# Performance work log

Measured on AMD Instinct MI355X. Metric: run time of the kernel, lower is better.

Reference implementation:

```python
import jax, jax.numpy as jnp
import numpy as np

B, S, DIM = 2, 2048, 1024
HID = 2048          # multiple_of-rounded hidden dim
E, NSH, TOPK = 8, 2, 2


def _ffn(x, w1, w2, w3):
    return (jax.nn.silu(x @ w1.T) * (x @ w3.T)) @ w2.T


def setup_inputs() -> dict:
    key = jax.random.key(0)
    ks = jax.random.split(key, 8)
    sc = 0.02  # init scale for stability
    return {
        "x": jax.random.normal(ks[0], (B, S, DIM), jnp.float32),
        "router_w": jax.random.normal(ks[1], (E, DIM), jnp.float32) * sc,
        "expert_bias": jnp.zeros((E,), jnp.float32),
        "w1": jax.random.normal(ks[2], (E, HID, DIM), jnp.float32) * sc,
        "w3": jax.random.normal(ks[3], (E, HID, DIM), jnp.float32) * sc,
        "w2": jax.random.normal(ks[4], (E, DIM, HID), jnp.float32) * sc,
        "sw1": jax.random.normal(ks[5], (NSH, HID, DIM), jnp.float32) * sc,
        "sw3": jax.random.normal(ks[6], (NSH, HID, DIM), jnp.float32) * sc,
        "sw2": jax.random.normal(ks[7], (NSH, DIM, HID), jnp.float32) * sc,
    }


def reference(x, router_w, expert_bias, w1, w3, w2, sw1, sw3, sw2):
    bs, sl, d = x.shape
    xf = x.reshape(-1, d)  # [T, d]

    # shared experts (always-on)
    shared = jnp.zeros_like(xf)
    for i in range(sw1.shape[0]):
        shared = shared + _ffn(xf, sw1[i], sw2[i], sw3[i])

    # router with aux-free load-balance bias
    logits = xf @ router_w.T + expert_bias  # [T, E]
    rw, sel = jax.lax.top_k(logits, TOPK)   # [T, K]
    rw = jax.nn.softmax(rw.astype(jnp.float32), axis=-1).astype(x.dtype)

    # combine weights per (token, expert): sum of routing weights over topk slots
    onehot = jax.nn.one_hot(sel, E, dtype=x.dtype)        # [T, K, E]
    combine = jnp.einsum('tk,tke->te', rw, onehot)        # [T, E]

    # per-expert FFN accumulated via scan (equivalent to gather-FFN-scatter)
    def body(acc, ew):
        e1, e3, e2, cw = ew  # cw: [T]
        acc = acc + cw[:, None] * _ffn(xf, e1, e2, e3)
        return acc, None

    out, _ = jax.lax.scan(body, jnp.zeros_like(xf), (w1, w3, w2, combine.T))
    out = out + shared
    return out.reshape(bs, sl, -1)
```

## Files before the change

### kernel.cpp

```cpp
#include <hip/hip_runtime.h>
#include <stdint.h>

#define T_TOK 4096
#define DIMD  1024
#define HIDN  2048
#define NEXP  8
#define RMAX  10240
#define RROWS (RMAX + 2 * T_TOK)

typedef float f32x4 __attribute__((ext_vector_type(4)));
typedef short s16x8 __attribute__((ext_vector_type(8)));

__device__ __forceinline__ uint16_t f2bf(float f) {
    uint32_t u = __builtin_bit_cast(uint32_t, f);
    u += 0x7fffu + ((u >> 16) & 1u);
    return (uint16_t)(u >> 16);
}
__device__ __forceinline__ float bf2f(uint32_t h) {
    return __builtin_bit_cast(float, h << 16);
}
__device__ __forceinline__ uint32_t pk2(float a, float b) {
    return (uint32_t)f2bf(a) | ((uint32_t)f2bf(b) << 16);
}
__device__ __forceinline__ void gload16(const void* g, void* l) {
    __builtin_amdgcn_global_load_lds(
        (const __attribute__((address_space(1))) void*)g,
        (__attribute__((address_space(3))) void*)l, 16, 0, 0);
}
#define BAR()        asm volatile("s_barrier" ::: "memory")
#define WAIT_VM4()   asm volatile("s_waitcnt vmcnt(4)" ::: "memory")
#define WAIT_VM0()   asm volatile("s_waitcnt vmcnt(0)" ::: "memory")
#define WAIT_LGKM0() asm volatile("s_waitcnt lgkmcnt(0)" ::: "memory")


struct CvtArgs {
    const float* s[7];
    uint16_t*    d[7];
    int          nq[7];
    int          mode[7];
};

__global__ void cvt_all_kernel(CvtArgs a) {
    int base = blockIdx.x * blockDim.x + threadIdx.x;
    int stride = gridDim.x * blockDim.x;
    #pragma unroll
    for (int seg = 0; seg < 7; ++seg) {
        const float4* sp = (const float4*)a.s[seg];
        uint2* dp = (uint2*)a.d[seg];
        int n = a.nq[seg];
        int mode = a.mode[seg];
        for (int i = base; i < n; i += stride) {
            float4 v = sp[i];
            uint2 o; o.x = pk2(v.x, v.y); o.y = pk2(v.z, v.w);
            int di = i;
            if (mode) {
                int e = i >> 19;
                int rem = i & 524287;
                int nr = rem >> 8;
                int kq = rem & 255;
                int np = ((nr >> 4) << 5) + ((mode == 2) ? 16 : 0) + (nr & 15);
                di = (e << 20) + (np << 8) + kq;
            }
            dp[di] = o;
        }
    }
}

__global__ __launch_bounds__(256)
void router_kernel(const float* __restrict__ x, const float* __restrict__ rw,
                   const float* __restrict__ bias,
                   int* __restrict__ sel, float* __restrict__ wgt,
                   int* __restrict__ cnt) {
    __shared__ float rws[NEXP * DIMD];
    int tid = threadIdx.x;
    for (int i = tid; i < NEXP * DIMD / 4; i += 256)
        ((float4*)rws)[i] = ((const float4*)rw)[i];
    __syncthreads();

    int wid = tid >> 6, lane = tid & 63;
    float b[NEXP];
    #pragma unroll
    for (int e = 0; e < NEXP; ++e) b[e] = bias[e];

    int t0 = (blockIdx.x * 4 + wid) * 8;
    for (int j = 0; j < 8; ++j) {
        int t = t0 + j;
        const float4* xr = (const float4*)(x + (size_t)t * DIMD);
        float p[NEXP] = {};
        #pragma unroll
        for (int c = 0; c < 4; ++c) {
            float4 xv = xr[c * 64 + lane];
            #pragma unroll
            for (int e = 0; e < NEXP; ++e) {
                float4 wv = *(const float4*)(rws + e * DIMD + c * 256 + lane * 4);
                p[e] += xv.x * wv.x + xv.y * wv.y + xv.z * wv.z + xv.w * wv.w;
            }
        }
        #pragma unroll
        for (int off = 32; off >= 1; off >>= 1) {
            #pragma unroll
            for (int e = 0; e < NEXP; ++e) p[e] += __shfl_xor(p[e], off, 64);
        }
        if (lane == 0) {
            #pragma unroll
            for (int e = 0; e < NEXP; ++e) p[e] += b[e];
            float l0 = -1e30f; int i0 = 0;
            #pragma unroll
            for (int e = 0; e < NEXP; ++e) { if (p[e] > l0) { l0 = p[e]; i0 = e; } }
            float l1 = -1e30f; int i1 = 0;
            #pragma unroll
            for (int e = 0; e < NEXP; ++e) { if (e == i0) continue; if (p[e] > l1) { l1 = p[e]; i1 = e; } }
            float e1 = expf(l1 - l0);
            float d = 1.f + e1;
            sel[t * 2] = i0; sel[t * 2 + 1] = i1;
            wgt[t * 2] = 1.f / d; wgt[t * 2 + 1] = e1 / d;
            atomicAdd(&cnt[i0], 1);
            atomicAdd(&cnt[i1], 1);
        }
    }
}

__global__ void offs_kernel(const int* __restrict__ cnt, int* __restrict__ offs) {
    if (threadIdx.x == 0 && blockIdx.x == 0) {
        int o = 0;
        for (int e = 0; e < NEXP; ++e) { offs[e] = o; o += (cnt[e] + 255) & ~255; }
        offs[NEXP] = o;
    }
}

__global__ void assign_kernel(const int* __restrict__ sel, const int* __restrict__ offs,
                              int* __restrict__ fill, int* __restrict__ row_of,
                              int* __restrict__ tok) {
    int i = blockIdx.x * blockDim.x + threadIdx.x;
    if (i < 2 * T_TOK) {
        int e = sel[i];
        int r = offs[e] + atomicAdd(&fill[e], 1);
        row_of[i] = r;
        tok[r] = i >> 1;
    } else if (i < 4 * T_TOK) {
        int j = i - 2 * T_TOK;
        tok[offs[NEXP] + j] = j & (T_TOK - 1);
    }
}

__global__ void combine_kernel(const uint16_t* __restrict__ H2, const int* __restrict__ row_of,
                               const float* __restrict__ wgt, const int* __restrict__ offs,
                               float* __restrict__ out) {
    int t = blockIdx.x;
    int c = threadIdx.x * 8;
    int r0 = row_of[t * 2], r1 = row_of[t * 2 + 1];
    int s0 = offs[NEXP] + t, s1 = s0 + T_TOK;
    float w0 = wgt[t * 2], w1 = wgt[t * 2 + 1];
    uint4 a = *(const uint4*)(H2 + (size_t)r0 * DIMD + c);
    uint4 b = *(const uint4*)(H2 + (size_t)r1 * DIMD + c);
    uint4 u = *(const uint4*)(H2 + (size_t)s0 * DIMD + c);
    uint4 v = *(const uint4*)(H2 + (size_t)s1 * DIMD + c);
    float4 o0, o1;
    o0.x = w0 * bf2f(a.x & 0xffffu) + w1 * bf2f(b.x & 0xffffu) + bf2f(u.x & 0xffffu) + bf2f(v.x & 0xffffu);
    o0.y = w0 * bf2f(a.x >> 16)     + w1 * bf2f(b.x >> 16)     + bf2f(u.x >> 16)     + bf2f(v.x >> 16);
    o0.z = w0 * bf2f(a.y & 0xffffu) + w1 * bf2f(b.y & 0xffffu) + bf2f(u.y & 0xffffu) + bf2f(v.y & 0xffffu);
    o0.w = w0 * bf2f(a.y >> 16)     + w1 * bf2f(b.y >> 16)     + bf2f(u.y >> 16)     + bf2f(v.y >> 16);
    o1.x = w0 * bf2f(a.z & 0xffffu) + w1 * bf2f(b.z & 0xffffu) + bf2f(u.z & 0xffffu) + bf2f(v.z & 0xffffu);
    o1.y = w0 * bf2f(a.z >> 16)     + w1 * bf2f(b.z >> 16)     + bf2f(u.z >> 16)     + bf2f(v.z >> 16);
    o1.z = w0 * bf2f(a.w & 0xffffu) + w1 * bf2f(b.w & 0xffffu) + bf2f(u.w & 0xffffu) + bf2f(v.w & 0xffffu);
    o1.w = w0 * bf2f(a.w >> 16)     + w1 * bf2f(b.w >> 16)     + bf2f(u.w >> 16)     + bf2f(v.w >> 16);
    float* o = out + (size_t)t * DIMD + c;
    *(float4*)o = o0;
    *(float4*)(o + 4) = o1;
}

__global__ __launch_bounds__(512, 2)
void gemm13_8p(const uint16_t* __restrict__ A, const int* __restrict__ tok,
               const uint16_t* __restrict__ W, uint16_t* __restrict__ H,
               const int* __restrict__ offs) {
    constexpr int K = DIMD;
    constexpr int NT = K / 64;
    __shared__ __align__(16) char lds[131072];

    int row0 = blockIdx.y * 256;
    int rsh = row0 - offs[NEXP];
    int e;
    if (rsh >= 0) {
        if (rsh >= 2 * T_TOK) return;
        e = NEXP + (rsh >> 12);
    } else {
        e = 0;
        while (row0 >= offs[e + 1]) ++e;
    }
    const uint16_t* wp = W + (size_t)e * (4096ull * 1024ull);
    int col0 = blockIdx.x * 256;

    int tid = threadIdx.x, lane = tid & 63, wid = tid >> 6;
    int wm = wid >> 2, wn = wid & 3;

    int sslot = (lane & 3) ^ ((tid >> 3) & 3);
    uint32_t aoff[2], boff[2];
    #pragma unroll
    for (int i = 0; i < 2; ++i) {
        int r = i * 128 + (tid >> 2);
        int garow = tok[row0 + r];
        aoff[i] = (uint32_t)garow * K + sslot * 8;
        boff[i] = (uint32_t)(col0 + r) * K + sslot * 8;
    }
    int ldsw = wid * 1024;

    int rslot = (((lane >> 4) ^ ((lane >> 1) & 3)) << 4);
    int aro = (wm * 128 + (lane & 15)) * 64 + rslot;
    int bro = (wn * 64 + (lane & 15)) * 64 + rslot;

    #define STAGE_A(buf, kt, ks) { \
        gload16(A + aoff[0] + (kt) + (ks) * 32, (buf) + (ks) * 16384 + ldsw); \
        gload16(A + aoff[1] + (kt) + (ks) * 32, (buf) + (ks) * 16384 + 8192 + ldsw); }
    #define STAGE_B(buf, kt, ks) { \
        gload16(wp + boff[0] + (kt) + (ks) * 32, (buf) + 32768 + (ks) * 16384 + ldsw); \
        gload16(wp + boff[1] + (kt) + (ks) * 32, (buf) + 32768 + (ks) * 16384 + 8192 + ldsw); }

    STAGE_A(lds, 0, 0); STAGE_B(lds, 0, 0);
    STAGE_A(lds, 0, 1); STAGE_B(lds, 0, 1);
    WAIT_VM4();
    BAR();

    f32x4 acc[8][4] = {};

    for (int t = 0; t < NT; ++t) {
        char* cur = lds + (t & 1) * 65536;
        char* nxt = lds + ((t + 1) & 1) * 65536;
        int kt1 = (t + 1) * 64;
        bool pre = (t + 1 < NT);
        s16x8 av[4], bv[4], av2[4];

        #pragma unroll
        for (int f = 0; f < 4; ++f) av[f] = *(const s16x8*)(cur + aro + f * 1024);
        #pragma unroll
        for (int f = 0; f < 4; ++f) bv[f] = *(const s16x8*)(cur + 32768 + bro + f * 1024);
        if (pre) STAGE_A(nxt, kt1, 0);
        BAR(); WAIT_LGKM0();
        __builtin_amdgcn_s_setprio(1);
        #pragma unroll
        for (int j = 0; j < 4; ++j)
            #pragma unroll
            for (int i = 0; i < 4; ++i)
                acc[i][j] = __builtin_amdgcn_mfma_f32_16x16x32_bf16(av[i], bv[j], acc[i][j], 0, 0, 0);
        __builtin_amdgcn_s_setprio(0);
        BAR();

        #pragma unroll
        for (int f = 0; f < 4; ++f) av2[f] = *(const s16x8*)(cur + aro + (f + 4) * 1024);
        if (pre) STAGE_B(nxt, kt1, 0);
        BAR(); WAIT_LGKM0();
        __builtin_amdgcn_s_setprio(1);
        #pragma unroll
        for (int j = 0; j < 4; ++j)
            #pragma unroll
            for (int i = 0; i < 4; ++i)
                acc[i + 4][j] = __builtin_amdgcn_mfma_f32_16x16x32_bf16(av2[i], bv[j], acc[i + 4][j], 0, 0, 0);
        __builtin_amdgcn_s_setprio(0);
        if (pre) { WAIT_VM4(); } else { WAIT_VM0(); }
        BAR();

        #pragma unroll
        for (int f = 0; f < 4; ++f) av[f] = *(const s16x8*)(cur + 16384 + aro + f * 1024);
        #pragma unroll
        for (int f = 0; f < 4; ++f) bv[f] = *(const s16x8*)(cur + 32768 + 16384 + bro + f * 1024);
        if (pre) STAGE_A(nxt, kt1, 1);
        BAR(); WAIT_LGKM0();
        __builtin_amdgcn_s_setprio(1);
        #pragma unroll
        for (int j = 0; j < 4; ++j)
            #pragma unroll
            for (int i = 0; i < 4; ++i)
                acc[i][j] = __builtin_amdgcn_mfma_f32_16x16x32_bf16(av[i], bv[j], acc[i][j], 0, 0, 0);
        __builtin_amdgcn_s_setprio(0);
        BAR();

        #pragma unroll
        for (int f = 0; f < 4; ++f) av2[f] = *(const s16x8*)(cur + 16384 + aro + (f + 4) * 1024);
        if (pre) STAGE_B(nxt, kt1, 1);
        BAR(); WAIT_LGKM0();
        __builtin_amdgcn_s_setprio(1);
        #pragma unroll
        for (int j = 0; j < 4; ++j)
            #pragma unroll
            for (int i = 0; i < 4; ++i)
                acc[i + 4][j] = __builtin_amdgcn_mfma_f32_16x16x32_bf16(av2[i], bv[j], acc[i + 4][j], 0, 0, 0);
        __builtin_amdgcn_s_setprio(0);
        if (pre) WAIT_VM4();
        BAR();
    }
    #undef STAGE_A
    #undef STAGE_B

    #pragma unroll
    for (int i = 0; i < 8; ++i) {
        int row = row0 + wm * 128 + i * 16 + ((lane >> 4) << 2);
        #pragma unroll
        for (int m = 0; m < 2; ++m) {
            int hc = ((col0 + wn * 64) >> 1) + m * 16 + (lane & 15);
            #pragma unroll
            for (int rg = 0; rg < 4; ++rg) {
                float a1 = acc[i][2 * m][rg];
                float a3 = acc[i][2 * m + 1][rg];
                float hv = (a1 / (1.f + __expf(-a1))) * a3;
                H[(size_t)(row + rg) * HIDN + hc] = f2bf(hv);
            }
        }
    }
}

__global__ __launch_bounds__(256, 2)
void gemm2_2p(const uint16_t* __restrict__ Hg,
              const uint16_t* __restrict__ W2, uint16_t* __restrict__ H2,
              const int* __restrict__ offs) {
    constexpr int K = HIDN;
    constexpr int NT = K / 64;
    __shared__ __align__(16) char lds[65536];

    int row0 = blockIdx.y * 128;
    int rsh = row0 - offs[NEXP];
    int e;
    if (rsh >= 0) {
        if (rsh >= 2 * T_TOK) return;
        e = NEXP + (rsh >> 12);
    } else {
        e = 0;
        while (row0 >= offs[e + 1]) ++e;
    }
    const uint16_t* wp = W2 + (size_t)e * DIMD * HIDN;
    int col0 = blockIdx.x * 128;

    int tid = threadIdx.x, lane = tid & 63, wid = tid >> 6;
    int wm = wid >> 1, wn = wid & 1;

    int chunk = (tid & 3) ^ ((tid >> 3) & 3);
    uint32_t aoff[2], boff[2];
    #pragma unroll
    for (int p = 0; p < 2; ++p) {
        int r = p * 64 + (tid >> 2);
        aoff[p] = (uint32_t)(row0 + r) * K + chunk * 8;
        boff[p] = (uint32_t)(col0 + r) * K + chunk * 8;
    }
    int ldsw = wid * 1024;

    int rslot = (((lane >> 4) ^ ((lane >> 1) & 3)) << 4);
    int aro = (wm * 64 + (lane & 15)) * 64 + rslot;
    int bro = (wn * 64 + (lane & 15)) * 64 + rslot + 16384;

    #define STG_A2(buf, kt, ks) { \
        gload16(Hg + aoff[0] + (kt) + (ks) * 32, (buf) + (ks) * 8192 + ldsw); \
        gload16(Hg + aoff[1] + (kt) + (ks) * 32, (buf) + (ks) * 8192 + 4096 + ldsw); }
    #define STG_B2(buf, kt, ks) { \
        gload16(wp + boff[0] + (kt) + (ks) * 32, (buf) + 16384 + (ks) * 8192 + ldsw); \
        gload16(wp + boff[1] + (kt) + (ks) * 32, (buf) + 16384 + (ks) * 8192 + 4096 + ldsw); }

    STG_A2(lds, 0, 0); STG_B2(lds, 0, 0);
    STG_A2(lds, 0, 1); STG_B2(lds, 0, 1);
    WAIT_VM4();
    BAR();

    f32x4 acc[4][4] = {};

    for (int t = 0; t < NT; ++t) {
        char* cur = lds + (t & 1) * 32768;
        char* nxt = lds + ((t + 1) & 1) * 32768;
        int kt1 = (t + 1) * 64;
        bool pre = (t + 1 < NT);
        s16x8 av[4], bv[4];

        #pragma unroll
        for (int f = 0; f < 4; ++f) av[f] = *(const s16x8*)(cur + aro + f * 1024);
        #pragma unroll
        for (int f = 0; f < 4; ++f) bv[f] = *(const s16x8*)(cur + bro + f * 1024);
        if (pre) { STG_A2(nxt, kt1, 0); STG_B2(nxt, kt1, 0); }
        BAR(); WAIT_LGKM0();
        __builtin_amdgcn_s_setprio(1);
        #pragma unroll
        for (int j = 0; j < 4; ++j)
            #pragma unroll
            for (int i = 0; i < 4; ++i)
                acc[i][j] = __builtin_amdgcn_mfma_f32_16x16x32_bf16(av[i], bv[j], acc[i][j], 0, 0, 0);
        __builtin_amdgcn_s_setprio(0);
        if (pre) { WAIT_VM4(); } else { WAIT_VM0(); }
        BAR();

        #pragma unroll
        for (int f = 0; f < 4; ++f) av[f] = *(const s16x8*)(cur + 8192 + aro + f * 1024);
        #pragma unroll
        for (int f = 0; f < 4; ++f) bv[f] = *(const s16x8*)(cur + 8192 + bro + f * 1024);
        if (pre) { STG_A2(nxt, kt1, 1); STG_B2(nxt, kt1, 1); }
        BAR(); WAIT_LGKM0();
        __builtin_amdgcn_s_setprio(1);
        #pragma unroll
        for (int j = 0; j < 4; ++j)
            #pragma unroll
            for (int i = 0; i < 4; ++i)
                acc[i][j] = __builtin_amdgcn_mfma_f32_16x16x32_bf16(av[i], bv[j], acc[i][j], 0, 0, 0);
        __builtin_amdgcn_s_setprio(0);
        if (pre) WAIT_VM4();
        BAR();
    }
    #undef STG_A2
    #undef STG_B2

    #pragma unroll
    for (int i = 0; i < 4; ++i) {
        #pragma unroll
        for (int j = 0; j < 4; ++j) {
            #pragma unroll
            for (int rg = 0; rg < 4; ++rg) {
                int row = row0 + wm * 64 + i * 16 + ((lane >> 4) << 2) + rg;
                int col = col0 + wn * 64 + j * 16 + (lane & 15);
                H2[(size_t)row * DIMD + col] = f2bf(acc[i][j][rg]);
            }
        }
    }
}


extern "C" void kernel_launch(void* const* d_in, const int* in_sizes, int n_in,
                              void* d_out, int out_size, void* d_ws, size_t ws_size,
                              hipStream_t stream) {
    const float* x   = (const float*)d_in[0];
    const float* rw  = (const float*)d_in[1];
    const float* eb  = (const float*)d_in[2];
    const float* w1  = (const float*)d_in[3];
    const float* w3  = (const float*)d_in[4];
    const float* w2  = (const float*)d_in[5];
    const float* sw1 = (const float*)d_in[6];
    const float* sw3 = (const float*)d_in[7];
    const float* sw2 = (const float*)d_in[8];
    float* out = (float*)d_out;

    const size_t EW = (size_t)NEXP * HIDN * DIMD;
    const size_t SW = (size_t)2 * HIDN * DIMD;

    char* ws = (char*)d_ws;
    size_t off = 0;
    auto alloc = [&](size_t b) { char* p = ws + off; off = (off + b + 255) & ~(size_t)255; return p; };
    uint16_t* xb    = (uint16_t*)alloc((size_t)T_TOK * DIMD * 2);
    uint16_t* Hg    = (uint16_t*)alloc((size_t)RROWS * HIDN * 2);
    uint16_t* H2    = (uint16_t*)alloc((size_t)RROWS * DIMD * 2);
    uint16_t* w13   = (uint16_t*)alloc((size_t)10 * 4096 * 1024 * 2);
    uint16_t* w2all = (uint16_t*)alloc((EW + SW) * 2);
    int*   sel    = (int*)  alloc(T_TOK * 2 * 4);
    float* wgt    = (float*)alloc(T_TOK * 2 * 4);
    int*   row_of = (int*)  alloc(T_TOK * 2 * 4);
    int*   tok    = (int*)  alloc(RROWS * 4);
    int*   cnt    = (int*)  alloc(64);
    int*   fill   = (int*)  alloc(64);
    int*   offs   = (int*)  alloc(64);

    hipMemsetAsync(cnt, 0, 64, stream);
    hipMemsetAsync(fill, 0, 64, stream);
    hipMemsetAsync(tok, 0, RROWS * 4, stream);

    CvtArgs ca;
    ca.s[0] = w1;  ca.d[0] = w13;                           ca.nq[0] = (int)(EW / 4); ca.mode[0] = 1;
    ca.s[1] = sw1; ca.d[1] = w13 + (size_t)8 * 4096 * 1024; ca.nq[1] = (int)(SW / 4); ca.mode[1] = 1;
    ca.s[2] = w3;  ca.d[2] = w13;                           ca.nq[2] = (int)(EW / 4); ca.mode[2] = 2;
    ca.s[3] = sw3; ca.d[3] = w13 + (size_t)8 * 4096 * 1024; ca.nq[3] = (int)(SW / 4); ca.mode[3] = 2;
    ca.s[4] = w2;  ca.d[4] = w2all;                         ca.nq[4] = (int)(EW / 4); ca.mode[4] = 0;
    ca.s[5] = sw2; ca.d[5] = w2all + EW;                    ca.nq[5] = (int)(SW / 4); ca.mode[5] = 0;
    ca.s[6] = x;   ca.d[6] = xb;                            ca.nq[6] = T_TOK * DIMD / 4; ca.mode[6] = 0;
    cvt_all_kernel<<<2048, 256, 0, stream>>>(ca);

    router_kernel<<<128, 256, 0, stream>>>(x, rw, eb, sel, wgt, cnt);
    offs_kernel<<<1, 1, 0, stream>>>(cnt, offs);
    assign_kernel<<<64, 256, 0, stream>>>(sel, offs, fill, row_of, tok);

    gemm13_8p<<<dim3(16, RROWS / 256), 512, 0, stream>>>(xb, tok, w13, Hg, offs);
    gemm2_2p<<<dim3(DIMD / 128, RROWS / 128), 256, 0, stream>>>(Hg, w2all, H2, offs);

    combine_kernel<<<T_TOK, 128, 0, stream>>>(H2, row_of, wgt, offs, out);
}
```

Measured before the change: 483.6 us.

## Switch both expert GEMMs to 4-stage 32-wide K ring-buffer pipeline

Result: slower. 495.4 us (+2.4%).

```diff
diff --git a/kernel.cpp b/kernel.cpp
--- a/kernel.cpp
+++ b/kernel.cpp
@@ -28,6 +28,7 @@
         (__attribute__((address_space(3))) void*)l, 16, 0, 0);
 }
 #define BAR()        asm volatile("s_barrier" ::: "memory")
+#define WAIT_VM8()   asm volatile("s_waitcnt vmcnt(8)" ::: "memory")
 #define WAIT_VM4()   asm volatile("s_waitcnt vmcnt(4)" ::: "memory")
 #define WAIT_VM0()   asm volatile("s_waitcnt vmcnt(0)" ::: "memory")
 #define WAIT_LGKM0() asm volatile("s_waitcnt lgkmcnt(0)" ::: "memory")
@@ -174,7 +175,7 @@
                const uint16_t* __restrict__ W, uint16_t* __restrict__ H,
                const int* __restrict__ offs) {
     constexpr int K = DIMD;
-    constexpr int NT = K / 64;
+    constexpr int NU = K / 32;
     __shared__ __align__(16) char lds[131072];
 
     int row0 = blockIdx.y * 256;
@@ -208,32 +209,33 @@
     int aro = (wm * 128 + (lane & 15)) * 64 + rslot;
     int bro = (wn * 64 + (lane & 15)) * 64 + rslot;
 
-    #define STAGE_A(buf, kt, ks) { \
-        gload16(A + aoff[0] + (kt) + (ks) * 32, (buf) + (ks) * 16384 + ldsw); \
-        gload16(A + aoff[1] + (kt) + (ks) * 32, (buf) + (ks) * 16384 + 8192 + ldsw); }
-    #define STAGE_B(buf, kt, ks) { \
-        gload16(wp + boff[0] + (kt) + (ks) * 32, (buf) + 32768 + (ks) * 16384 + ldsw); \
-        gload16(wp + boff[1] + (kt) + (ks) * 32, (buf) + 32768 + (ks) * 16384 + 8192 + ldsw); }
-
-    STAGE_A(lds, 0, 0); STAGE_B(lds, 0, 0);
-    STAGE_A(lds, 0, 1); STAGE_B(lds, 0, 1);
-    WAIT_VM4();
+    #define STAGE_A(buf, ku) { \
+        gload16(A + aoff[0] + (ku), (buf) + ldsw); \
+        gload16(A + aoff[1] + (ku), (buf) + 8192 + ldsw); }
+    #define STAGE_B(buf, ku) { \
+        gload16(wp + boff[0] + (ku), (buf) + 16384 + ldsw); \
+        gload16(wp + boff[1] + (ku), (buf) + 16384 + 8192 + ldsw); }
+
+    STAGE_A(lds, 0);                 STAGE_B(lds, 0);
+    STAGE_A(lds + 32768, 32);        STAGE_B(lds + 32768, 32);
+    STAGE_A(lds + 2 * 32768, 64);    STAGE_B(lds + 2 * 32768, 64);
+    WAIT_VM8();
     BAR();
 
     f32x4 acc[8][4] = {};
 
-    for (int t = 0; t < NT; ++t) {
-        char* cur = lds + (t & 1) * 65536;
-        char* nxt = lds + ((t + 1) & 1) * 65536;
-        int kt1 = (t + 1) * 64;
-        bool pre = (t + 1 < NT);
+    for (int u = 0; u < NU; ++u) {
+        char* cur = lds + (u & 3) * 32768;
+        char* nb  = lds + ((u + 3) & 3) * 32768;
+        int ku = (u + 3) * 32;
+        bool pre = (u + 3 < NU);
         s16x8 av[4], bv[4], av2[4];
 
         #pragma unroll
         for (int f = 0; f < 4; ++f) av[f] = *(const s16x8*)(cur + aro + f * 1024);
         #pragma unroll
-        for (int f = 0; f < 4; ++f) bv[f] = *(const s16x8*)(cur + 32768 + bro + f * 1024);
-        if (pre) STAGE_A(nxt, kt1, 0);
+        for (int f = 0; f < 4; ++f) bv[f] = *(const s16x8*)(cur + 16384 + bro + f * 1024);
+        if (pre) STAGE_A(nb, ku);
         BAR(); WAIT_LGKM0();
         __builtin_amdgcn_s_setprio(1);
         #pragma unroll
@@ -246,7 +248,7 @@
 
         #pragma unroll
         for (int f = 0; f < 4; ++f) av2[f] = *(const s16x8*)(cur + aro + (f + 4) * 1024);
-        if (pre) STAGE_B(nxt, kt1, 0);
+        if (pre) STAGE_B(nb, ku);
         BAR(); WAIT_LGKM0();
         __builtin_amdgcn_s_setprio(1);
         #pragma unroll
@@ -255,36 +257,9 @@
             for (int i = 0; i < 4; ++i)
                 acc[i + 4][j] = __builtin_amdgcn_mfma_f32_16x16x32_bf16(av2[i], bv[j], acc[i + 4][j], 0, 0, 0);
         __builtin_amdgcn_s_setprio(0);
-        if (pre) { WAIT_VM4(); } else { WAIT_VM0(); }
-        BAR();
-
-        #pragma unroll
-        for (int f = 0; f < 4; ++f) av[f] = *(const s16x8*)(cur + 16384 + aro + f * 1024);
-        #pragma unroll
-        for (int f = 0; f < 4; ++f) bv[f] = *(const s16x8*)(cur + 32768 + 16384 + bro + f * 1024);
-        if (pre) STAGE_A(nxt, kt1, 1);
-        BAR(); WAIT_LGKM0();
-        __builtin_amdgcn_s_setprio(1);
-        #pragma unroll
-        for (int j = 0; j < 4; ++j)
-            #pragma unroll
-            for (int i = 0; i < 4; ++i)
-                acc[i][j] = __builtin_amdgcn_mfma_f32_16x16x32_bf16(av[i], bv[j], acc[i][j], 0, 0, 0);
-        __builtin_amdgcn_s_setprio(0);
-        BAR();
-
-        #pragma unroll
-        for (int f = 0; f < 4; ++f) av2[f] = *(const s16x8*)(cur + 16384 + aro + (f + 4) * 1024);
-        if (pre) STAGE_B(nxt, kt1, 1);
-        BAR(); WAIT_LGKM0();
-        __builtin_amdgcn_s_setprio(1);
-        #pragma unroll
-        for (int j = 0; j < 4; ++j)
-            #pragma unroll
-            for (int i = 0; i < 4; ++i)
-                acc[i + 4][j] = __builtin_amdgcn_mfma_f32_16x16x32_bf16(av2[i], bv[j], acc[i + 4][j], 0, 0, 0);
-        __builtin_amdgcn_s_setprio(0);
-        if (pre) WAIT_VM4();
+        if (u <= NU - 4)      { WAIT_VM8(); }
+        else if (u == NU - 3) { WAIT_VM4(); }
+        else if (u == NU - 2) { WAIT_VM0(); }
         BAR();
     }
     #undef STAGE_A
@@ -312,7 +287,7 @@
               const uint16_t* __restrict__ W2, uint16_t* __restrict__ H2,
               const int* __restrict__ offs) {
     constexpr int K = HIDN;
-    constexpr int NT = K / 64;
+    constexpr int NU = K / 32;
     __shared__ __align__(16) char lds[65536];
 
     int row0 = blockIdx.y * 128;
@@ -343,34 +318,35 @@
 
     int rslot = (((lane >> 4) ^ ((lane >> 1) & 3)) << 4);
     int aro = (wm * 64 + (lane & 15)) * 64 + rslot;
-    int bro = (wn * 64 + (lane & 15)) * 64 + rslot + 16384;
-
-    #define STG_A2(buf, kt, ks) { \
-        gload16(Hg + aoff[0] + (kt) + (ks) * 32, (buf) + (ks) * 8192 + ldsw); \
-        gload16(Hg + aoff[1] + (kt) + (ks) * 32, (buf) + (ks) * 8192 + 4096 + ldsw); }
-    #define STG_B2(buf, kt, ks) { \
-        gload16(wp + boff[0] + (kt) + (ks) * 32, (buf) + 16384 + (ks) * 8192 + ldsw); \
-        gload16(wp + boff[1] + (kt) + (ks) * 32, (buf) + 16384 + (ks) * 8192 + 4096 + ldsw); }
-
-    STG_A2(lds, 0, 0); STG_B2(lds, 0, 0);
-    STG_A2(lds, 0, 1); STG_B2(lds, 0, 1);
-    WAIT_VM4();
+    int bro = (wn * 64 + (lane & 15)) * 64 + rslot;
+
+    #define STG_A2(buf, ku) { \
+        gload16(Hg + aoff[0] + (ku), (buf) + ldsw); \
+        gload16(Hg + aoff[1] + (ku), (buf) + 4096 + ldsw); }
+    #define STG_B2(buf, ku) { \
+        gload16(wp + boff[0] + (ku), (buf) + 8192 + ldsw); \
+        gload16(wp + boff[1] + (ku), (buf) + 8192 + 4096 + ldsw); }
+
+    STG_A2(lds, 0);                STG_B2(lds, 0);
+    STG_A2(lds + 16384, 32);       STG_B2(lds + 16384, 32);
+    STG_A2(lds + 2 * 16384, 64);   STG_B2(lds + 2 * 16384, 64);
+    WAIT_VM8();
     BAR();
 
     f32x4 acc[4][4] = {};
 
-    for (int t = 0; t < NT; ++t) {
-        char* cur = lds + (t & 1) * 32768;
-        char* nxt = lds + ((t + 1) & 1) * 32768;
-        int kt1 = (t + 1) * 64;
-        bool pre = (t + 1 < NT);
+    for (int u = 0; u < NU; ++u) {
+        char* cur = lds + (u & 3) * 16384;
+        char* nb  = lds + ((u + 3) & 3) * 16384;
+        int ku = (u + 3) * 32;
+        bool pre = (u + 3 < NU);
         s16x8 av[4], bv[4];
 
         #pragma unroll
         for (int f = 0; f < 4; ++f) av[f] = *(const s16x8*)(cur + aro + f * 1024);
         #pragma unroll
-        for (int f = 0; f < 4; ++f) bv[f] = *(const s16x8*)(cur + bro + f * 1024);
-        if (pre) { STG_A2(nxt, kt1, 0); STG_B2(nxt, kt1, 0); }
+        for (int f = 0; f < 4; ++f) bv[f] = *(const s16x8*)(cur + 8192 + bro + f * 1024);
+        if (pre) { STG_A2(nb, ku); STG_B2(nb, ku); }
         BAR(); WAIT_LGKM0();
         __builtin_amdgcn_s_setprio(1);
         #pragma unroll
@@ -379,23 +355,9 @@
             for (int i = 0; i < 4; ++i)
                 acc[i][j] = __builtin_amdgcn_mfma_f32_16x16x32_bf16(av[i], bv[j], acc[i][j], 0, 0, 0);
         __builtin_amdgcn_s_setprio(0);
-        if (pre) { WAIT_VM4(); } else { WAIT_VM0(); }
-        BAR();
-
-        #pragma unroll
-        for (int f = 0; f < 4; ++f) av[f] = *(const s16x8*)(cur + 8192 + aro + f * 1024);
-        #pragma unroll
-        for (int f = 0; f < 4; ++f) bv[f] = *(const s16x8*)(cur + 8192 + bro + f * 1024);
-        if (pre) { STG_A2(nxt, kt1, 1); STG_B2(nxt, kt1, 1); }
-        BAR(); WAIT_LGKM0();
-        __builtin_amdgcn_s_setprio(1);
-        #pragma unroll
-        for (int j = 0; j < 4; ++j)
-            #pragma unroll
-            for (int i = 0; i < 4; ++i)
-                acc[i][j] = __builtin_amdgcn_mfma_f32_16x16x32_bf16(av[i], bv[j], acc[i][j], 0, 0, 0);
-        __builtin_amdgcn_s_setprio(0);
-        if (pre) WAIT_VM4();
+        if (u <= NU - 4)      { WAIT_VM8(); }
+        else if (u == NU - 3) { WAIT_VM4(); }
+        else if (u == NU - 2) { WAIT_VM0(); }
         BAR();
     }
     #undef STG_A2
```
